# Optimization experiments

Measured on AMD Instinct MI355X. Metric: run time of the kernel, lower is better.

The kernel has to match this reference:

```python
import jax, jax.numpy as jnp
import numpy as np

B, S, D, W, L = 16, 2048, 256, 8, 3


def _ln(x, g, b):
    # LayerNorm as in annotated-transformer SublayerConnection (eps=1e-6)
    m = jnp.mean(x, axis=-1, keepdims=True)
    v = jnp.var(x, axis=-1, keepdims=True)
    return g * (x - m) / jnp.sqrt(v + 1e-6) + b


def _ffn(x, w1, b1, w2, b2):
    # PositionwiseFeedForward: w2(relu(w1(x))), dropout off in eval
    return jax.nn.relu(x @ w1 + b1) @ w2 + b2


def setup_inputs() -> dict:
    key = jax.random.key(0)
    ks = jax.random.split(key, 16)
    s = 0.05
    inp = {
        "inputs": jax.random.normal(ks[0], (B, S, D), jnp.float32),
        "left_padding": jax.random.normal(ks[1], (W, D), jnp.float32) * s,
        "right_padding": jax.random.normal(ks[2], (W, D), jnp.float32) * s,
        "left_weights": jax.random.normal(ks[3], (W + 1,), jnp.float32) / (W + 1),
        "right_weights": jax.random.normal(ks[4], (W + 1,), jnp.float32) / (W + 1),
        "left_w1": jax.random.normal(ks[5], (L, D, D), jnp.float32) * s,
        "left_b1": jnp.zeros((L, D), jnp.float32),
        "left_w2": jax.random.normal(ks[6], (L, D, D), jnp.float32) * s,
        "left_b2": jnp.zeros((L, D), jnp.float32),
        "left_ln_g": jnp.ones((L, D), jnp.float32),
        "left_ln_b": jnp.zeros((L, D), jnp.float32),
        "right_w1": jax.random.normal(ks[7], (L, D, D), jnp.float32) * s,
        "right_b1": jnp.zeros((L, D), jnp.float32),
        "right_w2": jax.random.normal(ks[8], (L, D, D), jnp.float32) * s,
        "right_b2": jnp.zeros((L, D), jnp.float32),
        "right_ln_g": jnp.ones((L, D), jnp.float32),
        "right_ln_b": jnp.zeros((L, D), jnp.float32),
    }
    return inp


def reference(inputs, left_padding, right_padding, left_weights, right_weights,
              left_w1, left_b1, left_w2, left_b2, left_ln_g, left_ln_b,
              right_w1, right_b1, right_w2, right_b2, right_ln_g, right_ln_b):
    b, s, d = inputs.shape
    w = left_padding.shape[0]
    nl = left_w1.shape[0]
    # pad with learned boundary vectors: (b, w + s + w, d)
    padded = jnp.concatenate([
        jnp.broadcast_to(left_padding, (b, w, d)),
        inputs,
        jnp.broadcast_to(right_padding, (b, w, d)),
    ], axis=1)
    # vectorized unfold replacing the per-position python loop:
    idx = jnp.arange(s)[:, None] + jnp.arange(w + 1)[None, :]  # (s, w+1)
    left_win = padded[:, idx]        # (b, s, w+1, d): tokens t-w .. t
    right_win = padded[:, idx + w]   # (b, s, w+1, d): tokens t .. t+w
    left_out = jnp.einsum('bswd,w->bsd', left_win, left_weights)
    right_out = jnp.einsum('bswd,w->bsd', right_win, right_weights)
    layers = []
    for i in range(nl):
        # SublayerConnection: x + FFN(LN(x))
        left_out = left_out + _ffn(_ln(left_out, left_ln_g[i], left_ln_b[i]),
                                   left_w1[i], left_b1[i], left_w2[i], left_b2[i])
        right_out = right_out + _ffn(_ln(right_out, right_ln_g[i], right_ln_b[i]),
                                     right_w1[i], right_b1[i], right_w2[i], right_b2[i])
        layers.append(jnp.concatenate([left_out, right_out], axis=-1))  # (b, s, 2d)
    all_layers = jnp.stack(layers, axis=0)  # (nl, b, s, 2d)
    return all_layers, layers[-1]
```

## Files before the change

kernel.cpp:

```cpp
#include <hip/hip_runtime.h>

typedef __attribute__((ext_vector_type(8))) short bf16x8;
typedef __attribute__((ext_vector_type(4))) float f32x4;

#define UR _Pragma("unroll")

__device__ __forceinline__ float bf2f(unsigned short u) {
    union { unsigned int i; float f; } v; v.i = ((unsigned int)u) << 16; return v.f;
}
__device__ __forceinline__ unsigned short f2bf(float f) {
    union { float f; unsigned int i; } v; v.f = f;
    unsigned int u = v.i;
    return (unsigned short)((u + 0x7FFFu + ((u >> 16) & 1u)) >> 16);
}
__device__ __forceinline__ uint2 pack4(f32x4 x) {
    uint2 o;
    o.x = (unsigned int)f2bf(x[0]) | ((unsigned int)f2bf(x[1]) << 16);
    o.y = (unsigned int)f2bf(x[2]) | ((unsigned int)f2bf(x[3]) << 16);
    return o;
}
__device__ __forceinline__ int swz(int r, int c) {
    return r * 512 + (c ^ ((r & 7) << 4));
}

__global__ __launch_bounds__(256)
void prep_kernel(const float* __restrict__ lw1, const float* __restrict__ rw1,
                 const float* __restrict__ lw2, const float* __restrict__ rw2,
                 unsigned short* __restrict__ w1t, unsigned short* __restrict__ w2t)
{
    int t = blockIdx.x * 256 + threadIdx.x;
    int tensor = t / 196608;
    int e = t - tensor * 196608;
    int l = e >> 16, rem = e & 65535;
    int n = rem >> 8, k = rem & 255;
    const float* src = (tensor == 0) ? lw1 : (tensor == 1) ? rw1 : (tensor == 2) ? lw2 : rw2;
    unsigned short* dst = ((tensor < 2) ? w1t : w2t) + (tensor & 1) * 196608;
    dst[e] = f2bf(src[(l << 16) + (k << 8) + n]);
}

__global__ __launch_bounds__(256)
void conv_kernel(const float* __restrict__ inp,
                 const float* __restrict__ lpad, const float* __restrict__ rpad,
                 const float* __restrict__ lwt, const float* __restrict__ rwt,
                 uint2* __restrict__ wsL, uint2* __restrict__ wsR)
{
    int idx = blockIdx.x * 256 + threadIdx.x;
    int r = idx >> 6, d4 = idx & 63;
    int s = r & 2047;
    int c = d4 * 4;
    f32x4 aL = {0.f, 0.f, 0.f, 0.f}, aR = {0.f, 0.f, 0.f, 0.f};
    UR for (int j = -8; j <= 8; ++j) {
        int i = s + j;
        const float* src;
        if (i < 0)          src = lpad + (i + 8) * 256 + c;
        else if (i >= 2048) src = rpad + (i - 2048) * 256 + c;
        else                src = inp + (size_t)(r + j) * 256 + c;
        f32x4 v = *(const f32x4*)src;
        if (j <= 0) { float w = lwt[j + 8]; aL += v * w; }
        if (j >= 0) { float w = rwt[j];     aR += v * w; }
    }
    wsL[idx] = pack4(aL);
    wsR[idx] = pack4(aR);
}

__global__ __launch_bounds__(512, 2)
void mega_kernel(const unsigned short* __restrict__ convbf,
                 const unsigned short* __restrict__ w1t,
                 const unsigned short* __restrict__ w2t,
                 const float* __restrict__ b1L, const float* __restrict__ b1R,
                 const float* __restrict__ b2L, const float* __restrict__ b2R,
                 const float* __restrict__ gL,  const float* __restrict__ gR,
                 const float* __restrict__ bbL, const float* __restrict__ bbR,
                 float* __restrict__ out)
{
    __shared__ unsigned short YH[128 * 256];
    __shared__ float red[4][128][2];

    const int tid = threadIdx.x;
    const int wv = tid >> 6;
    const int ln = tid & 63;
    const int lr = ln & 15;
    const int lh = ln >> 4;
    const int wm = wv >> 1;
    const int wn = wv & 1;

    const int bid  = blockIdx.x;
    const int br   = bid >> 8;
    const int tile = bid & 255;
    const int r0   = tile * 128;

    const unsigned short* cv  = convbf + (size_t)br * (32768u * 256u);
    const unsigned short* W1b = w1t + (size_t)br * 196608;
    const unsigned short* W2b = w2t + (size_t)br * 196608;
    const float* B1 = br ? b1R : b1L;
    const float* B2 = br ? b2R : b2L;
    const float* G  = br ? gR  : gL;
    const float* Bb = br ? bbR : bbL;

    int rr[4], dd[4], hh[4];
    UR for (int n = 0; n < 4; ++n) rr[n] = wn * 64 + n * 16 + lr;
    UR for (int m = 0; m < 4; ++m) dd[m] = wm * 64 + m * 16 + lh * 4;
    UR for (int m = 0; m < 4; ++m) hh[m] = wm * 64 + m * 16 + lr;

    f32x4 x[4][4];
    UR for (int m = 0; m < 4; ++m)
      UR for (int n = 0; n < 4; ++n) {
        uint2 raw = *(const uint2*)(cv + (size_t)(r0 + rr[n]) * 256 + dd[m]);
        f32x4 v;
        v[0] = bf2f((unsigned short)(raw.x & 0xffffu));
        v[1] = bf2f((unsigned short)(raw.x >> 16));
        v[2] = bf2f((unsigned short)(raw.y & 0xffffu));
        v[3] = bf2f((unsigned short)(raw.y >> 16));
        x[m][n] = v;
      }

    for (int lay = 0; lay < 3; ++lay) {
        UR for (int n = 0; n < 4; ++n) {
            float s = 0.f, q = 0.f;
            UR for (int m = 0; m < 4; ++m)
              UR for (int r = 0; r < 4; ++r) { float v = x[m][n][r]; s += v; q += v * v; }
            s += __shfl_xor(s, 16); q += __shfl_xor(q, 16);
            s += __shfl_xor(s, 32); q += __shfl_xor(q, 32);
            if (lh == 0) {
                red[wm][wn * 64 + n * 16 + lr][0] = s;
                red[wm][wn * 64 + n * 16 + lr][1] = q;
            }
        }
        __syncthreads();
        float mean[4], rstd[4];
        UR for (int n = 0; n < 4; ++n) {
            int row = wn * 64 + n * 16 + lr;
            float S = 0.f, Q = 0.f;
            UR for (int w = 0; w < 4; ++w) { S += red[w][row][0]; Q += red[w][row][1]; }
            float mu = S * (1.f / 256.f);
            float var = Q * (1.f / 256.f) - mu * mu;
            mean[n] = mu;
            rstd[n] = rsqrtf(var + 1e-6f);
        }
        f32x4 gf[4], bfr_[4];
        UR for (int m = 0; m < 4; ++m) {
            gf[m]   = *(const f32x4*)(G  + lay * 256 + dd[m]);
            bfr_[m] = *(const f32x4*)(Bb + lay * 256 + dd[m]);
        }
        UR for (int m = 0; m < 4; ++m)
          UR for (int n = 0; n < 4; ++n) {
            f32x4 y;
            UR for (int r = 0; r < 4; ++r)
                y[r] = (x[m][n][r] - mean[n]) * rstd[n] * gf[m][r] + bfr_[m][r];
            *(uint2*)((char*)YH + swz(rr[n], dd[m] * 2)) = pack4(y);
          }
        __syncthreads();

        const unsigned short* Wl = W1b + lay * 65536;
        f32x4 acc[4][4];
        UR for (int m = 0; m < 4; ++m)
          UR for (int n = 0; n < 4; ++n) acc[m][n] = (f32x4){0.f, 0.f, 0.f, 0.f};
        UR for (int kk = 0; kk < 8; ++kk) {
            bf16x8 a[4], b[4];
            UR for (int m = 0; m < 4; ++m)
                a[m] = *(const bf16x8*)(Wl + hh[m] * 256 + kk * 32 + lh * 8);
            UR for (int n = 0; n < 4; ++n)
                b[n] = *(const bf16x8*)((const char*)YH + swz(rr[n], kk * 64 + lh * 16));
            UR for (int m = 0; m < 4; ++m)
              UR for (int n = 0; n < 4; ++n)
                acc[m][n] = __builtin_amdgcn_mfma_f32_16x16x32_bf16(a[m], b[n], acc[m][n], 0, 0, 0);
        }
        f32x4 b1f[4];
        UR for (int m = 0; m < 4; ++m) b1f[m] = *(const f32x4*)(B1 + lay * 256 + dd[m]);
        __syncthreads();
        UR for (int m = 0; m < 4; ++m)
          UR for (int n = 0; n < 4; ++n) {
            f32x4 h;
            UR for (int r = 0; r < 4; ++r) h[r] = fmaxf(acc[m][n][r] + b1f[m][r], 0.f);
            *(uint2*)((char*)YH + swz(rr[n], dd[m] * 2)) = pack4(h);
          }
        __syncthreads();

        const unsigned short* W2l = W2b + lay * 65536;
        UR for (int m = 0; m < 4; ++m)
          UR for (int n = 0; n < 4; ++n) acc[m][n] = (f32x4){0.f, 0.f, 0.f, 0.f};
        UR for (int kk = 0; kk < 8; ++kk) {
            bf16x8 a[4], b[4];
            UR for (int m = 0; m < 4; ++m)
                a[m] = *(const bf16x8*)(W2l + hh[m] * 256 + kk * 32 + lh * 8);
            UR for (int n = 0; n < 4; ++n)
                b[n] = *(const bf16x8*)((const char*)YH + swz(rr[n], kk * 64 + lh * 16));
            UR for (int m = 0; m < 4; ++m)
              UR for (int n = 0; n < 4; ++n)
                acc[m][n] = __builtin_amdgcn_mfma_f32_16x16x32_bf16(a[m], b[n], acc[m][n], 0, 0, 0);
        }
        f32x4 b2f[4];
        UR for (int m = 0; m < 4; ++m) b2f[m] = *(const f32x4*)(B2 + lay * 256 + dd[m]);
        UR for (int m = 0; m < 4; ++m)
          UR for (int n = 0; n < 4; ++n)
            UR for (int r = 0; r < 4; ++r)
                x[m][n][r] += acc[m][n][r] + b2f[m][r];

        float* outL = out + ((size_t)lay * 32768 + r0) * 512 + br * 256;
        UR for (int m = 0; m < 4; ++m)
          UR for (int n = 0; n < 4; ++n) {
            float* p = outL + (size_t)rr[n] * 512 + dd[m];
            *(f32x4*)p = x[m][n];
            if (lay == 2) *(f32x4*)(p + 16777216) = x[m][n];
          }
    }
}

extern "C" void kernel_launch(void* const* d_in, const int* in_sizes, int n_in,
                              void* d_out, int out_size, void* d_ws, size_t ws_size,
                              hipStream_t stream)
{
    const float* inputs = (const float*)d_in[0];
    const float* lpad = (const float*)d_in[1];
    const float* rpad = (const float*)d_in[2];
    const float* lwt  = (const float*)d_in[3];
    const float* rwt  = (const float*)d_in[4];
    const float* lw1  = (const float*)d_in[5];
    const float* lb1  = (const float*)d_in[6];
    const float* lw2  = (const float*)d_in[7];
    const float* lb2  = (const float*)d_in[8];
    const float* lg   = (const float*)d_in[9];
    const float* lbb  = (const float*)d_in[10];
    const float* rw1  = (const float*)d_in[11];
    const float* rb1  = (const float*)d_in[12];
    const float* rw2  = (const float*)d_in[13];
    const float* rb2  = (const float*)d_in[14];
    const float* rg   = (const float*)d_in[15];
    const float* rbb  = (const float*)d_in[16];

    char* ws = (char*)d_ws;
    unsigned short* convb = (unsigned short*)ws;
    unsigned short* w1t   = (unsigned short*)(ws + 33554432);
    unsigned short* w2t   = (unsigned short*)(ws + 33554432 + 786432);

    prep_kernel<<<3072, 256, 0, stream>>>(lw1, rw1, lw2, rw2, w1t, w2t);
    conv_kernel<<<8192, 256, 0, stream>>>(inputs, lpad, rpad, lwt, rwt,
                                          (uint2*)convb, (uint2*)(convb + 32768u * 256u));
    mega_kernel<<<512, 512, 0, stream>>>(convb, w1t, w2t,
                                         lb1, rb1, lb2, rb2, lg, rg, lbb, rbb,
                                         (float*)d_out);
}
```

Before: 528.7 us.

## Retile mega kernel to 32-row blocks, reuse conv loads, tile weight transpose

```diff
diff --git a/kernel.cpp b/kernel.cpp
--- a/kernel.cpp
+++ b/kernel.cpp
@@ -28,42 +28,72 @@
                  const float* __restrict__ lw2, const float* __restrict__ rw2,
                  unsigned short* __restrict__ w1t, unsigned short* __restrict__ w2t)
 {
-    int t = blockIdx.x * 256 + threadIdx.x;
-    int tensor = t / 196608;
-    int e = t - tensor * 196608;
-    int l = e >> 16, rem = e & 65535;
-    int n = rem >> 8, k = rem & 255;
+    __shared__ unsigned short T[64][68];
+    int bid = blockIdx.x;
+    int mat = bid >> 4;
+    int tile = bid & 15;
+    int tensor = mat / 3;
+    int l = mat - tensor * 3;
+    int k0 = (tile >> 2) * 64, n0 = (tile & 3) * 64;
     const float* src = (tensor == 0) ? lw1 : (tensor == 1) ? rw1 : (tensor == 2) ? lw2 : rw2;
     unsigned short* dst = ((tensor < 2) ? w1t : w2t) + (tensor & 1) * 196608;
-    dst[e] = f2bf(src[(l << 16) + (k << 8) + n]);
-}
-
-__global__ __launch_bounds__(256)
+
+    int tx = threadIdx.x & 63, ty = threadIdx.x >> 6;
+    UR for (int p = 0; p < 16; ++p) {
+        int k = k0 + p * 4 + ty;
+        T[tx][k - k0] = f2bf(src[l * 65536 + k * 256 + n0 + tx]);
+    }
+    __syncthreads();
+    UR for (int p = 0; p < 16; ++p) {
+        int n = n0 + p * 4 + ty;
+        dst[l * 65536 + n * 256 + k0 + tx] = T[n - n0][tx];
+    }
+}
+
+__global__ __launch_bounds__(256, 4)
 void conv_kernel(const float* __restrict__ inp,
                  const float* __restrict__ lpad, const float* __restrict__ rpad,
                  const float* __restrict__ lwt, const float* __restrict__ rwt,
                  uint2* __restrict__ wsL, uint2* __restrict__ wsR)
 {
-    int idx = blockIdx.x * 256 + threadIdx.x;
-    int r = idx >> 6, d4 = idx & 63;
-    int s = r & 2047;
-    int c = d4 * 4;
-    f32x4 aL = {0.f, 0.f, 0.f, 0.f}, aR = {0.f, 0.f, 0.f, 0.f};
-    UR for (int j = -8; j <= 8; ++j) {
-        int i = s + j;
+    int raw = blockIdx.x;
+    int w = (raw & 7) * 128 + (raw >> 3);
+    int t = threadIdx.x;
+    int q = t & 63;
+    int g = t >> 6;
+    int R0 = w * 32 + g * 8;
+    int s0 = R0 & 2047;
+    int c = q * 4;
+
+    float wl[9], wr[9];
+    UR for (int j = 0; j < 9; ++j) { wl[j] = lwt[j]; wr[j] = rwt[j]; }
+
+    f32x4 aL[8], aR[8];
+    UR for (int k = 0; k < 8; ++k) {
+        aL[k] = (f32x4){0.f, 0.f, 0.f, 0.f};
+        aR[k] = (f32x4){0.f, 0.f, 0.f, 0.f};
+    }
+    UR for (int i = -8; i <= 15; ++i) {
+        int si = s0 + i;
         const float* src;
-        if (i < 0)          src = lpad + (i + 8) * 256 + c;
-        else if (i >= 2048) src = rpad + (i - 2048) * 256 + c;
-        else                src = inp + (size_t)(r + j) * 256 + c;
+        if (si < 0)          src = lpad + (si + 8) * 256 + c;
+        else if (si >= 2048) src = rpad + (si - 2048) * 256 + c;
+        else                 src = inp + (size_t)(R0 + i) * 256 + c;
         f32x4 v = *(const f32x4*)src;
-        if (j <= 0) { float w = lwt[j + 8]; aL += v * w; }
-        if (j >= 0) { float w = rwt[j];     aR += v * w; }
-    }
-    wsL[idx] = pack4(aL);
-    wsR[idx] = pack4(aR);
-}
-
-__global__ __launch_bounds__(512, 2)
+        UR for (int k = 0; k < 8; ++k) {
+            int j = i - k;
+            if (j >= -8 && j <= 0) aL[k] += v * wl[j + 8];
+            if (j >= 0 && j <= 8)  aR[k] += v * wr[j];
+        }
+    }
+    UR for (int k = 0; k < 8; ++k) {
+        int idx = (R0 + k) * 64 + q;
+        wsL[idx] = pack4(aL[k]);
+        wsR[idx] = pack4(aR[k]);
+    }
+}
+
+__global__ __launch_bounds__(256, 4)
 void mega_kernel(const unsigned short* __restrict__ convbf,
                  const unsigned short* __restrict__ w1t,
                  const unsigned short* __restrict__ w2t,
@@ -73,21 +103,20 @@
                  const float* __restrict__ bbL, const float* __restrict__ bbR,
                  float* __restrict__ out)
 {
-    __shared__ unsigned short YH[128 * 256];
-    __shared__ float red[4][128][2];
-
-    const int tid = threadIdx.x;
-    const int wv = tid >> 6;
-    const int ln = tid & 63;
+    __shared__ unsigned short YH[32 * 256];
+    __shared__ float red[4][32][2];
+
+    const int t = threadIdx.x;
+    const int wm = t >> 6;
+    const int ln = t & 63;
     const int lr = ln & 15;
     const int lh = ln >> 4;
-    const int wm = wv >> 1;
-    const int wn = wv & 1;
-
-    const int bid  = blockIdx.x;
-    const int br   = bid >> 8;
-    const int tile = bid & 255;
-    const int r0   = tile * 128;
+
+    const int raw = blockIdx.x;
+    const int w = (raw & 7) * 256 + (raw >> 3);
+    const int br = w >> 10;
+    const int tile = w & 1023;
+    const int r0 = tile * 32;
 
     const unsigned short* cv  = convbf + (size_t)br * (32768u * 256u);
     const unsigned short* W1b = w1t + (size_t)br * 196608;
@@ -97,41 +126,41 @@
     const float* G  = br ? gR  : gL;
     const float* Bb = br ? bbR : bbL;
 
-    int rr[4], dd[4], hh[4];
-    UR for (int n = 0; n < 4; ++n) rr[n] = wn * 64 + n * 16 + lr;
+    int rr[2], dd[4], hh[4];
+    UR for (int n = 0; n < 2; ++n) rr[n] = n * 16 + lr;
     UR for (int m = 0; m < 4; ++m) dd[m] = wm * 64 + m * 16 + lh * 4;
     UR for (int m = 0; m < 4; ++m) hh[m] = wm * 64 + m * 16 + lr;
 
-    f32x4 x[4][4];
+    f32x4 x[4][2];
     UR for (int m = 0; m < 4; ++m)
-      UR for (int n = 0; n < 4; ++n) {
-        uint2 raw = *(const uint2*)(cv + (size_t)(r0 + rr[n]) * 256 + dd[m]);
+      UR for (int n = 0; n < 2; ++n) {
+        uint2 raw2 = *(const uint2*)(cv + (size_t)(r0 + rr[n]) * 256 + dd[m]);
         f32x4 v;
-        v[0] = bf2f((unsigned short)(raw.x & 0xffffu));
-        v[1] = bf2f((unsigned short)(raw.x >> 16));
-        v[2] = bf2f((unsigned short)(raw.y & 0xffffu));
-        v[3] = bf2f((unsigned short)(raw.y >> 16));
+        v[0] = bf2f((unsigned short)(raw2.x & 0xffffu));
+        v[1] = bf2f((unsigned short)(raw2.x >> 16));
+        v[2] = bf2f((unsigned short)(raw2.y & 0xffffu));
+        v[3] = bf2f((unsigned short)(raw2.y >> 16));
         x[m][n] = v;
       }
 
     for (int lay = 0; lay < 3; ++lay) {
-        UR for (int n = 0; n < 4; ++n) {
+        UR for (int n = 0; n < 2; ++n) {
             float s = 0.f, q = 0.f;
             UR for (int m = 0; m < 4; ++m)
               UR for (int r = 0; r < 4; ++r) { float v = x[m][n][r]; s += v; q += v * v; }
             s += __shfl_xor(s, 16); q += __shfl_xor(q, 16);
             s += __shfl_xor(s, 32); q += __shfl_xor(q, 32);
             if (lh == 0) {
-                red[wm][wn * 64 + n * 16 + lr][0] = s;
-                red[wm][wn * 64 + n * 16 + lr][1] = q;
+                red[wm][n * 16 + lr][0] = s;
+                red[wm][n * 16 + lr][1] = q;
             }
         }
         __syncthreads();
-        float mean[4], rstd[4];
-        UR for (int n = 0; n < 4; ++n) {
-            int row = wn * 64 + n * 16 + lr;
+        float mean[2], rstd[2];
+        UR for (int n = 0; n < 2; ++n) {
+            int row = n * 16 + lr;
             float S = 0.f, Q = 0.f;
-            UR for (int w = 0; w < 4; ++w) { S += red[w][row][0]; Q += red[w][row][1]; }
+            UR for (int u = 0; u < 4; ++u) { S += red[u][row][0]; Q += red[u][row][1]; }
             float mu = S * (1.f / 256.f);
             float var = Q * (1.f / 256.f) - mu * mu;
             mean[n] = mu;
@@ -143,7 +172,7 @@
             bfr_[m] = *(const f32x4*)(Bb + lay * 256 + dd[m]);
         }
         UR for (int m = 0; m < 4; ++m)
-          UR for (int n = 0; n < 4; ++n) {
+          UR for (int n = 0; n < 2; ++n) {
             f32x4 y;
             UR for (int r = 0; r < 4; ++r)
                 y[r] = (x[m][n][r] - mean[n]) * rstd[n] * gf[m][r] + bfr_[m][r];
@@ -152,24 +181,24 @@
         __syncthreads();
 
         const unsigned short* Wl = W1b + lay * 65536;
-        f32x4 acc[4][4];
-        UR for (int m = 0; m < 4; ++m)
-          UR for (int n = 0; n < 4; ++n) acc[m][n] = (f32x4){0.f, 0.f, 0.f, 0.f};
+        f32x4 acc[4][2];
+        UR for (int m = 0; m < 4; ++m)
+          UR for (int n = 0; n < 2; ++n) acc[m][n] = (f32x4){0.f, 0.f, 0.f, 0.f};
         UR for (int kk = 0; kk < 8; ++kk) {
-            bf16x8 a[4], b[4];
+            bf16x8 a[4], b[2];
             UR for (int m = 0; m < 4; ++m)
                 a[m] = *(const bf16x8*)(Wl + hh[m] * 256 + kk * 32 + lh * 8);
-            UR for (int n = 0; n < 4; ++n)
+            UR for (int n = 0; n < 2; ++n)
                 b[n] = *(const bf16x8*)((const char*)YH + swz(rr[n], kk * 64 + lh * 16));
             UR for (int m = 0; m < 4; ++m)
-              UR for (int n = 0; n < 4; ++n)
+              UR for (int n = 0; n < 2; ++n)
                 acc[m][n] = __builtin_amdgcn_mfma_f32_16x16x32_bf16(a[m], b[n], acc[m][n], 0, 0, 0);
         }
         f32x4 b1f[4];
         UR for (int m = 0; m < 4; ++m) b1f[m] = *(const f32x4*)(B1 + lay * 256 + dd[m]);
         __syncthreads();
         UR for (int m = 0; m < 4; ++m)
-          UR for (int n = 0; n < 4; ++n) {
+          UR for (int n = 0; n < 2; ++n) {
             f32x4 h;
             UR for (int r = 0; r < 4; ++r) h[r] = fmaxf(acc[m][n][r] + b1f[m][r], 0.f);
             *(uint2*)((char*)YH + swz(rr[n], dd[m] * 2)) = pack4(h);
@@ -178,27 +207,27 @@
 
         const unsigned short* W2l = W2b + lay * 65536;
         UR for (int m = 0; m < 4; ++m)
-          UR for (int n = 0; n < 4; ++n) acc[m][n] = (f32x4){0.f, 0.f, 0.f, 0.f};
+          UR for (int n = 0; n < 2; ++n) acc[m][n] = (f32x4){0.f, 0.f, 0.f, 0.f};
         UR for (int kk = 0; kk < 8; ++kk) {
-            bf16x8 a[4], b[4];
+            bf16x8 a[4], b[2];
             UR for (int m = 0; m < 4; ++m)
                 a[m] = *(const bf16x8*)(W2l + hh[m] * 256 + kk * 32 + lh * 8);
-            UR for (int n = 0; n < 4; ++n)
+            UR for (int n = 0; n < 2; ++n)
                 b[n] = *(const bf16x8*)((const char*)YH + swz(rr[n], kk * 64 + lh * 16));
             UR for (int m = 0; m < 4; ++m)
-              UR for (int n = 0; n < 4; ++n)
+              UR for (int n = 0; n < 2; ++n)
                 acc[m][n] = __builtin_amdgcn_mfma_f32_16x16x32_bf16(a[m], b[n], acc[m][n], 0, 0, 0);
         }
         f32x4 b2f[4];
         UR for (int m = 0; m < 4; ++m) b2f[m] = *(const f32x4*)(B2 + lay * 256 + dd[m]);
         UR for (int m = 0; m < 4; ++m)
-          UR for (int n = 0; n < 4; ++n)
+          UR for (int n = 0; n < 2; ++n)
             UR for (int r = 0; r < 4; ++r)
                 x[m][n][r] += acc[m][n][r] + b2f[m][r];
 
         float* outL = out + ((size_t)lay * 32768 + r0) * 512 + br * 256;
         UR for (int m = 0; m < 4; ++m)
-          UR for (int n = 0; n < 4; ++n) {
+          UR for (int n = 0; n < 2; ++n) {
             float* p = outL + (size_t)rr[n] * 512 + dd[m];
             *(f32x4*)p = x[m][n];
             if (lay == 2) *(f32x4*)(p + 16777216) = x[m][n];
@@ -233,10 +262,10 @@
     unsigned short* w1t   = (unsigned short*)(ws + 33554432);
     unsigned short* w2t   = (unsigned short*)(ws + 33554432 + 786432);
 
-    prep_kernel<<<3072, 256, 0, stream>>>(lw1, rw1, lw2, rw2, w1t, w2t);
-    conv_kernel<<<8192, 256, 0, stream>>>(inputs, lpad, rpad, lwt, rwt,
+    prep_kernel<<<192, 256, 0, stream>>>(lw1, rw1, lw2, rw2, w1t, w2t);
+    conv_kernel<<<1024, 256, 0, stream>>>(inputs, lpad, rpad, lwt, rwt,
                                           (uint2*)convb, (uint2*)(convb + 32768u * 256u));
-    mega_kernel<<<512, 512, 0, stream>>>(convb, w1t, w2t,
-                                         lb1, rb1, lb2, rb2, lg, rg, lbb, rbb,
-                                         (float*)d_out);
-}
+    mega_kernel<<<2048, 256, 0, stream>>>(convb, w1t, w2t,
+                                          lb1, rb1, lb2, rb2, lg, rg, lbb, rbb,
+                                          (float*)d_out);
+}
```

New measurement: 550.7 us. 1.04x slower.
